# Kernel optimization log

Hardware: AMD Instinct MI355X
Metric: run time of the kernel (lower is better)

The kernel has to match this reference:

```python
import jax, jax.numpy as jnp
import numpy as np

B, C, H_IMG, W_IMG = 8, 256, 32, 32
KS, VS, NH = 64, 64, 8
DIM_HEAD = KS * NH  # 512
S = H_IMG * W_IMG   # 1024


def _conv1x1(x, w, b):
    # x: (B, Cin, H, W), w: (Cout, Cin), b: (Cout,)
    return jnp.einsum('oc,bchw->bohw', w, x) + b[None, :, None, None]


def _gated_resnet(x, w1, b1, w2, b2):
    # kernel_size=1, no aux/cond/norm/dropout -> conv1(elu(x)); elu; conv2; GLU; +x
    h = _conv1x1(jax.nn.elu(x), w1, b1)
    h = _conv1x1(jax.nn.elu(h), w2, b2)
    a, g = jnp.split(h, 2, axis=1)
    return x + a * jax.nn.sigmoid(g)


def _branch(x, w1, b1, w2, b2, wn, bn):
    # GatedResNet followed by nin (1x1 linear over channels)
    return _conv1x1(_gated_resnet(x, w1, b1, w2, b2), wn, bn)


def setup_inputs() -> dict:
    key = jax.random.key(0)
    ks = jax.random.split(key, 16)
    d = {}
    d['query'] = jax.random.normal(ks[0], (B, C, H_IMG, W_IMG), jnp.float32)
    d['key'] = jax.random.normal(ks[1], (B, C, H_IMG, W_IMG), jnp.float32)
    i = 2
    for p, out_dim in [('q', DIM_HEAD), ('k', DIM_HEAD), ('v', VS * NH)]:
        d[f'{p}_gr_w1'] = jax.random.normal(ks[i], (C, C), jnp.float32) * 0.05; i += 1
        d[f'{p}_gr_b1'] = jnp.zeros((C,), jnp.float32)
        d[f'{p}_gr_w2'] = jax.random.normal(ks[i], (2 * C, C), jnp.float32) * 0.05; i += 1
        d[f'{p}_gr_b2'] = jnp.zeros((2 * C,), jnp.float32)
        d[f'{p}_nin_w'] = jax.random.normal(ks[i], (out_dim, C), jnp.float32) * 0.05; i += 1
        d[f'{p}_nin_b'] = jnp.zeros((out_dim,), jnp.float32)
    return d


def reference(query, key,
              q_gr_w1, q_gr_b1, q_gr_w2, q_gr_b2, q_nin_w, q_nin_b,
              k_gr_w1, k_gr_b1, k_gr_w2, k_gr_b2, k_nin_w, k_nin_b,
              v_gr_w1, v_gr_b1, v_gr_w2, v_gr_b2, v_nin_w, v_nin_b):
    b, _, h, w = key.shape
    s = h * w
    q = _branch(query, q_gr_w1, q_gr_b1, q_gr_w2, q_gr_b2, q_nin_w, q_nin_b)  # (B, NH*KS, H, W)
    v = _branch(key, v_gr_w1, v_gr_b1, v_gr_w2, v_gr_b2, v_nin_w, v_nin_b)    # (B, NH*VS, H, W)
    k = _branch(key, k_gr_w1, k_gr_b1, k_gr_w2, k_gr_b2, k_nin_w, k_nin_b)    # (B, NH*KS, H, W)

    # Faithful to torch .view on contiguous NCHW (row-major reshape mixes C and HW)
    q = q.reshape(b, -1, NH, KS).swapaxes(1, 2)          # (B, NH, S, KS)
    k = k.reshape(b, -1, NH, KS).transpose(0, 2, 3, 1)   # (B, NH, KS, S)
    v = v.reshape(b, -1, NH, VS).swapaxes(1, 2)          # (B, NH, S, VS)

    attn = jnp.matmul(q, k) / jnp.sqrt(jnp.float32(DIM_HEAD))  # (B, NH, S, S)
    # mask = triu(ones, k=1).T -> strictly lower triangular allowed (diagonal masked)
    allowed = jnp.tril(jnp.ones((s, s), bool), k=-1)
    attn = jnp.where(allowed, attn, jnp.float32(-10000.0))
    attn = jax.nn.softmax(attn, axis=3)
    # start_mask zeros out the first query row
    start_mask = jnp.ones((s, 1), jnp.float32).at[0, 0].set(0.0)
    attn = attn * start_mask

    out = jnp.matmul(attn, v)                 # (B, NH, S, VS)
    out = out.swapaxes(1, 2).reshape(b, h, w, VS * NH)
    out = out.transpose(0, 3, 1, 2)           # (B, VS*NH, H, W)
    return out
```

## Files before the change

kernel.cpp:

```cpp
#include <hip/hip_runtime.h>
#include <cstdint>
#include <cstddef>

typedef __attribute__((ext_vector_type(4))) float f32x4;
typedef __attribute__((ext_vector_type(8))) short bf16x8;
typedef __attribute__((ext_vector_type(4))) short bf16x4;
typedef __attribute__((ext_vector_type(2))) short bf16x2;

#define DEVI static __device__ __forceinline__

DEVI short f2bf(float f){
  union { float f; uint32_t u; } v; v.f = f;
  uint32_t r = v.u + 0x7FFFu + ((v.u >> 16) & 1u);
  return (short)(r >> 16);
}
DEVI float bf2f(short h){
  union { uint32_t u; float f; } v; v.u = ((uint32_t)(uint16_t)h) << 16;
  return v.f;
}
DEVI float eluf(float x){ return x > 0.f ? x : (__expf(x) - 1.f); }
DEVI float sigm(float x){ return 1.f / (1.f + __expf(-x)); }

static constexpr int NPIX = 8 * 1024;

static constexpr size_t SZ_W   = (size_t)983040 * 2;
static constexpr size_t SZ_ACT = (size_t)NPIX * 256 * 2;
static constexpr size_t OFF_W   = 0;
static constexpr size_t OFF_TOK = OFF_W + SZ_W + 8*SZ_ACT;

__global__ void k_prep(const float* __restrict__ w1q, const float* __restrict__ w2q, const float* __restrict__ wnq,
                       const float* __restrict__ w1k, const float* __restrict__ w2k, const float* __restrict__ wnk,
                       const float* __restrict__ w1v, const float* __restrict__ w2v, const float* __restrict__ wnv,
                       short* __restrict__ dst)
{
  const float* s1[3] = {w1q, w1k, w1v};
  const float* s2[3] = {w2q, w2k, w2v};
  const float* s3[3] = {wnq, wnk, wnv};
  const int stride = gridDim.x * blockDim.x;
  for (int i = blockIdx.x * blockDim.x + threadIdx.x; i < 983040; i += stride){
    int br = i / 327680;
    int r  = i - br * 327680;
    float v;
    if (r < 65536)        v = s1[br][r];
    else if (r < 196608)  v = s2[br][r - 65536];
    else                  v = s3[br][r - 196608];
    dst[i] = f2bf(v);
  }
}

DEVI const short* stage_ptr(const short* W1z, int s, int& r0){
  if (s < 8){ r0 = s << 5; return W1z; }
  if (s < 24){ int t = s - 8; r0 = ((t & 2) << 7) + ((t >> 2) << 6) + ((t & 1) << 5); return W1z + 65536; }
  int t = s - 24; r0 = t << 5; return W1z + 196608;
}

__global__ __launch_bounds__(256, 2)
void k_branch(const short* __restrict__ wsW,
              const float* __restrict__ query, const float* __restrict__ key,
              const float* __restrict__ b1q, const float* __restrict__ b1k, const float* __restrict__ b1v,
              const float* __restrict__ b2q, const float* __restrict__ b2k, const float* __restrict__ b2v,
              const float* __restrict__ bnq, const float* __restrict__ bnk, const float* __restrict__ bnv,
              short* __restrict__ tok)
{
  __shared__ short sW[2][8192];
  __shared__ short sHG[4][4096];

  const int z = blockIdx.y;
  const float* xin = (z == 0) ? query : key;
  const float* b1z = (z == 0) ? b1q : ((z == 1) ? b1k : b1v);
  const float* b2z = (z == 0) ? b2q : ((z == 1) ? b2k : b2v);
  const float* bnz = (z == 0) ? bnq : ((z == 1) ? bnk : bnv);
  const short* W1 = wsW + (size_t)z * 327680;
  short* tokz = tok + (size_t)z * NPIX * 512;

  const int tid = threadIdx.x, w = tid >> 6, g = (tid >> 4) & 3, li = tid & 15;
  const int gtok = blockIdx.x * 64 + w * 16;
  const int b = gtok >> 10, s0 = gtok & 1023;
  short* sHw = &sHG[w][0];
  const float* xb = xin + (size_t)b * 256 * 1024;

  bf16x8 stg[4];
#define STAGE_ISSUE(SN)                                                         \
  { int r0_; const short* Wb_ = stage_ptr(W1, (SN), r0_);                       \
    _Pragma("unroll")                                                           \
    for (int it = 0; it < 4; it++){                                             \
      int gi = tid + it*256;                                                    \
      stg[it] = *(const bf16x8*)(Wb_ + (size_t)(r0_ + (gi >> 5))*256 + ((gi & 31) << 3)); } }
#define STAGE_WRITE(BUF)                                                        \
  { _Pragma("unroll")                                                           \
    for (int it = 0; it < 4; it++){                                             \
      int gi = tid + it*256; int row = gi >> 5;                                 \
      *(bf16x8*)((BUF) + row*256 + ((((gi & 31) ^ (row & 7))) << 3)) = stg[it]; } }

  STAGE_ISSUE(0);
  STAGE_WRITE(sW[0]);

  bf16x8 bB[8];
  #pragma unroll
  for (int ks = 0; ks < 8; ks++){
    #pragma unroll
    for (int j = 0; j < 8; j++){
      float e = xb[(size_t)(ks*32 + g*8 + j)*1024 + s0 + li];
      bB[ks][j] = f2bf(eluf(e));
    }
  }

  for (int s = 0; s < 8; s++){
    __syncthreads();
    STAGE_ISSUE(s + 1);
    const short* bufc = sW[s & 1];
    f32x4 acc[2] = {};
    #pragma unroll
    for (int mt = 0; mt < 2; mt++)
      #pragma unroll
      for (int ks = 0; ks < 8; ks++){
        bf16x8 afr = *(const bf16x8*)(bufc + (mt*16 + li)*256 + (((ks*4 + g) ^ (li & 7)) << 3));
        acc[mt] = __builtin_amdgcn_mfma_f32_16x16x32_bf16(afr, bB[ks], acc[mt], 0, 0, 0);
      }
    #pragma unroll
    for (int mt = 0; mt < 2; mt++){
      int m0 = s*32 + mt*16 + g*4;
      bf16x4 pk;
      #pragma unroll
      for (int r = 0; r < 4; r++)
        pk[r] = f2bf(eluf(acc[mt][r] + b1z[m0 + r]));
      *(bf16x4*)(sHw + li*256 + (m0 ^ ((li & 7) << 3))) = pk;
    }
    STAGE_WRITE(sW[(s + 1) & 1]);
  }

  bf16x8 bH[8];
  #pragma unroll
  for (int ks = 0; ks < 8; ks++)
    bH[ks] = *(const bf16x8*)(sHw + li*256 + (((ks*4 + g) ^ (li & 7)) << 3));

  for (int mp = 0; mp < 4; mp++){
    f32x4 acc8[8] = {};
    #pragma unroll
    for (int q = 0; q < 4; q++){
      const int s = 8 + mp*4 + q;
      __syncthreads();
      STAGE_ISSUE(s + 1);
      const short* bufc = sW[s & 1];
      #pragma unroll
      for (int mt = 0; mt < 2; mt++)
        #pragma unroll
        for (int ks = 0; ks < 8; ks++){
          bf16x8 afr = *(const bf16x8*)(bufc + (mt*16 + li)*256 + (((ks*4 + g) ^ (li & 7)) << 3));
          acc8[q*2 + mt] = __builtin_amdgcn_mfma_f32_16x16x32_bf16(afr, bH[ks], acc8[q*2 + mt], 0, 0, 0);
        }
      STAGE_WRITE(sW[(s + 1) & 1]);
    }
    #pragma unroll
    for (int mt = 0; mt < 4; mt++){
      int m0 = mp*64 + mt*16 + g*4;
      bf16x4 pk;
      #pragma unroll
      for (int r = 0; r < 4; r++){
        float a  = acc8[mt][r] + b2z[m0 + r];
        float gg = acc8[4 + mt][r] + b2z[m0 + r + 256];
        float xv = xb[(size_t)(m0 + r)*1024 + s0 + li];
        pk[r] = f2bf(xv + a * sigm(gg));
      }
      *(bf16x4*)(sHw + li*256 + (m0 ^ ((li & 7) << 3))) = pk;
    }
  }

  bf16x8 bG[8];
  #pragma unroll
  for (int ks = 0; ks < 8; ks++)
    bG[ks] = *(const bf16x8*)(sHw + li*256 + (((ks*4 + g) ^ (li & 7)) << 3));

  for (int s3 = 0; s3 < 16; s3++){
    const int s = 24 + s3;
    __syncthreads();
    const int sn = (s + 1 < 40) ? (s + 1) : 39;
    STAGE_ISSUE(sn);
    const short* bufc = sW[s & 1];
    f32x4 acc[2] = {};
    #pragma unroll
    for (int mt = 0; mt < 2; mt++)
      #pragma unroll
      for (int ks = 0; ks < 8; ks++){
        bf16x8 afr = *(const bf16x8*)(bufc + (mt*16 + li)*256 + (((ks*4 + g) ^ (li & 7)) << 3));
        acc[mt] = __builtin_amdgcn_mfma_f32_16x16x32_bf16(afr, bG[ks], acc[mt], 0, 0, 0);
      }
    #pragma unroll
    for (int mt = 0; mt < 2; mt++){
      #pragma unroll
      for (int r = 0; r < 4; r++){
        int m = s3*32 + mt*16 + g*4 + r;
        tokz[((size_t)b*512 + m)*1024 + s0 + li] = f2bf(acc[mt][r] + bnz[m]);
      }
    }
    STAGE_WRITE(sW[(s + 1) & 1]);
  }
#undef STAGE_ISSUE
#undef STAGE_WRITE
}

__global__ void k_attn(const short* __restrict__ tok, float* __restrict__ out)
{
  const short* qtok = tok;
  const short* ktok = tok + (size_t)NPIX * 512;
  const short* vtok = tok + (size_t)2 * NPIX * 512;
  const int flat = blockIdx.x;
  const int p = flat >> 6;
  const int g4 = p >> 2, r4 = p & 3;
  const int qt = (g4 == 0) ? (15 - r4) : (g4 == 1) ? r4 : (g4 == 2) ? (11 - r4) : (4 + r4);
  const int bh = flat & 63;
  const int b = bh >> 3, nh = bh & 7;
  const int tid = threadIdx.x, lane = tid & 63, w = tid >> 6, g = (tid >> 4) & 3, li = tid & 15;
  const int qrow = qt*64 + w*16 + li;
  __shared__ short Kl[64*64];
  __shared__ short Vt[64*64];
  __shared__ short Pl[4][1024];

  const short* qptr = qtok + ((size_t)(b*1024 + qrow))*512 + nh*64;
  bf16x8 qf0 = *(const bf16x8*)(qptr + g*8);
  bf16x8 qf1 = *(const bf16x8*)(qptr + 32 + g*8);

  f32x4 accO[4] = {};
  float mrun = -1e30f, lrun = 0.f;
  const float scale = 0.04419417382415922f;
  short* Pw = &Pl[w][0];

  for (int kt = 0; kt <= qt; kt++){
    const int kb = kt * 64;
    __syncthreads();
    #pragma unroll
    for (int it = 0; it < 2; it++){
      int i = tid + it*256;
      int kr = i >> 3, kc = i & 7;
      bf16x8 v = *(const bf16x8*)(ktok + ((size_t)(b*1024 + kb + kr))*512 + nh*64 + kc*8);
      *(bf16x8*)(Kl + ((kr*64 + kc*8) ^ ((kr & 7) << 3))) = v;
    }
    #pragma unroll
    for (int it = 0; it < 2; it++){
      int d0 = w*8 + it*32;
      bf16x8 v = *(const bf16x8*)(vtok + ((size_t)(b*1024 + kb + lane))*512 + nh*64 + d0);
      #pragma unroll
      for (int j = 0; j < 8; j++){
        int d = d0 + j;
        Vt[(d*64 + lane) ^ ((d & 7) << 3)] = v[j];
      }
    }
    __syncthreads();

    float pv[16];
    float mt_ = -1e30f;
    const bool diag = (kt == qt);
    #pragma unroll
    for (int kf = 0; kf < 4; kf++){
      f32x4 sa = {};
      const int krow = kf*16 + li;
      bf16x8 ka  = *(const bf16x8*)(Kl + ((krow*64 + g*8) ^ ((krow & 7) << 3)));
      bf16x8 kbf = *(const bf16x8*)(Kl + ((krow*64 + 32 + g*8) ^ ((krow & 7) << 3)));
      sa = __builtin_amdgcn_mfma_f32_16x16x32_bf16(ka, qf0, sa, 0, 0, 0);
      sa = __builtin_amdgcn_mfma_f32_16x16x32_bf16(kbf, qf1, sa, 0, 0, 0);
      #pragma unroll
      for (int r = 0; r < 4; r++){
        const int keyg = kb + kf*16 + g*4 + r;
        float s = sa[r] * scale;
        const bool ok = (!diag) || (keyg < qrow);
        s = ok ? s : -1e30f;
        pv[kf*4 + r] = s;
        mt_ = fmaxf(mt_, s);
      }
    }
    mt_ = fmaxf(mt_, __shfl_xor(mt_, 16));
    mt_ = fmaxf(mt_, __shfl_xor(mt_, 32));
    const float mnew = fmaxf(mrun, mt_);
    const float alpha = __expf(mrun - mnew);
    short pr[16];
    float rs = 0.f;
    #pragma unroll
    for (int i2 = 0; i2 < 16; i2++){
      float p2 = (pv[i2] > -9e29f) ? __expf(pv[i2] - mnew) : 0.f;
      short pb = f2bf(p2);
      pr[i2] = pb;
      rs += bf2f(pb);
    }
    rs += __shfl_xor(rs, 16);
    rs += __shfl_xor(rs, 32);
    lrun = lrun * alpha + rs;
    mrun = mnew;
    #pragma unroll
    for (int df = 0; df < 4; df++){
      accO[df][0] *= alpha; accO[df][1] *= alpha;
      accO[df][2] *= alpha; accO[df][3] *= alpha;
    }
    #pragma unroll
    for (int kf = 0; kf < 4; kf++){
      #pragma unroll
      for (int rp = 0; rp < 2; rp++){
        bf16x2 two;
        two[0] = pr[kf*4 + rp*2];
        two[1] = pr[kf*4 + rp*2 + 1];
        const int key = kf*16 + g*4 + rp*2;
        *(bf16x2*)(Pw + ((li*64 + key) ^ ((li & 7) << 3))) = two;
      }
    }
    #pragma unroll
    for (int kc = 0; kc < 2; kc++){
      bf16x8 pf = *(const bf16x8*)(Pw + ((li*64 + kc*32 + g*8) ^ ((li & 7) << 3)));
      #pragma unroll
      for (int df = 0; df < 4; df++){
        const int dr = df*16 + li;
        bf16x8 vf = *(const bf16x8*)(Vt + ((dr*64 + kc*32 + g*8) ^ ((dr & 7) << 3)));
        accO[df] = __builtin_amdgcn_mfma_f32_16x16x32_bf16(vf, pf, accO[df], 0, 0, 0);
      }
    }
  }
  const float inv = (lrun > 0.f) ? (1.f / lrun) : 0.f;
  #pragma unroll
  for (int df = 0; df < 4; df++){
    #pragma unroll
    for (int r = 0; r < 4; r++){
      const int d = df*16 + g*4 + r;
      out[((size_t)b*512 + nh*64 + d)*1024 + qrow] = accO[df][r] * inv;
    }
  }
}

extern "C" void kernel_launch(void* const* d_in, const int* in_sizes, int n_in,
                              void* d_out, int out_size, void* d_ws, size_t ws_size,
                              hipStream_t stream)
{
  (void)in_sizes; (void)n_in; (void)out_size; (void)ws_size;
  const float* query = (const float*)d_in[0];
  const float* key   = (const float*)d_in[1];
  const float* w1[3] = {(const float*)d_in[2],  (const float*)d_in[8],  (const float*)d_in[14]};
  const float* b1[3] = {(const float*)d_in[3],  (const float*)d_in[9],  (const float*)d_in[15]};
  const float* w2[3] = {(const float*)d_in[4],  (const float*)d_in[10], (const float*)d_in[16]};
  const float* b2[3] = {(const float*)d_in[5],  (const float*)d_in[11], (const float*)d_in[17]};
  const float* wn[3] = {(const float*)d_in[6],  (const float*)d_in[12], (const float*)d_in[18]};
  const float* bn[3] = {(const float*)d_in[7],  (const float*)d_in[13], (const float*)d_in[19]};

  char* ws = (char*)d_ws;
  short* wsW = (short*)(ws + OFF_W);
  short* tok = (short*)(ws + OFF_TOK);
  float* out = (float*)d_out;

  k_prep<<<dim3(960), dim3(256), 0, stream>>>(w1[0], w2[0], wn[0],
                                              w1[1], w2[1], wn[1],
                                              w1[2], w2[2], wn[2], wsW);
  k_branch<<<dim3(128, 3), dim3(256), 0, stream>>>(wsW, query, key,
                                                   b1[0], b1[1], b1[2],
                                                   b2[0], b2[1], b2[2],
                                                   bn[0], bn[1], bn[2], tok);
  k_attn<<<dim3(1024), dim3(256), 0, stream>>>(tok, out);
}
```

Before: 81.05 us.

## Double tokens per wave in branch kernel and stream weights via global_load_lds

k_prep now writes weights pre-ordered by stage and pre-swizzled, so k_branch can copy each stage straight from global memory into LDS with global_load_lds, with no register staging. Each wave now handles 32 tokens instead of 16, so every weight fragment read from LDS feeds two MFMAs. This halves weight traffic per token and the grid shrinks to 64x3 blocks. In exchange there is more LDS and register use (launch bounds drop to 1 block per SM), fewer blocks to keep the GPU busy, and the barrier placement is reordered.

```diff
diff --git a/kernel.cpp b/kernel.cpp
--- a/kernel.cpp
+++ b/kernel.cpp
@@ -20,6 +20,11 @@
 }
 DEVI float eluf(float x){ return x > 0.f ? x : (__expf(x) - 1.f); }
 DEVI float sigm(float x){ return 1.f / (1.f + __expf(-x)); }
+
+DEVI void gload16(const void* g, void* l){
+  __builtin_amdgcn_global_load_lds((const __attribute__((address_space(1))) void*)g,
+                                   (__attribute__((address_space(3))) void*)l, 16, 0, 0);
+}
 
 static constexpr int NPIX = 8 * 1024;
 
@@ -36,25 +41,23 @@
   const float* s1[3] = {w1q, w1k, w1v};
   const float* s2[3] = {w2q, w2k, w2v};
   const float* s3[3] = {wnq, wnk, wnv};
-  const int stride = gridDim.x * blockDim.x;
-  for (int i = blockIdx.x * blockDim.x + threadIdx.x; i < 983040; i += stride){
-    int br = i / 327680;
-    int r  = i - br * 327680;
-    float v;
-    if (r < 65536)        v = s1[br][r];
-    else if (r < 196608)  v = s2[br][r - 65536];
-    else                  v = s3[br][r - 196608];
-    dst[i] = f2bf(v);
-  }
-}
-
-DEVI const short* stage_ptr(const short* W1z, int s, int& r0){
-  if (s < 8){ r0 = s << 5; return W1z; }
-  if (s < 24){ int t = s - 8; r0 = ((t & 2) << 7) + ((t >> 2) << 6) + ((t & 1) << 5); return W1z + 65536; }
-  int t = s - 24; r0 = t << 5; return W1z + 196608;
-}
-
-__global__ __launch_bounds__(256, 2)
+  int u = blockIdx.x * 256 + threadIdx.x;
+  if (u >= 122880) return;
+  int z = u / 40960, rem = u % 40960;
+  int stage = rem >> 10, rem2 = rem & 1023;
+  int r = rem2 >> 5, s_ = rem2 & 31;
+  int cslot = s_ ^ (r & 7);
+  const float* src; int row;
+  if (stage < 8){ src = s1[z]; row = stage*32 + r; }
+  else if (stage < 24){ int t = stage - 8; src = s2[z]; row = ((t&2)<<7) + ((t>>2)<<6) + ((t&1)<<5) + r; }
+  else { src = s3[z]; row = (stage-24)*32 + r; }
+  const float* p = src + (size_t)row*256 + cslot*8;
+  short* dq = dst + (size_t)u*8;
+  #pragma unroll
+  for (int e = 0; e < 8; e++) dq[e] = f2bf(p[e]);
+}
+
+__global__ __launch_bounds__(256, 1)
 void k_branch(const short* __restrict__ wsW,
               const float* __restrict__ query, const float* __restrict__ key,
               const float* __restrict__ b1q, const float* __restrict__ b1k, const float* __restrict__ b1v,
@@ -63,140 +66,149 @@
               short* __restrict__ tok)
 {
   __shared__ short sW[2][8192];
-  __shared__ short sHG[4][4096];
+  __shared__ short sHG[4][8192];
 
   const int z = blockIdx.y;
   const float* xin = (z == 0) ? query : key;
   const float* b1z = (z == 0) ? b1q : ((z == 1) ? b1k : b1v);
   const float* b2z = (z == 0) ? b2q : ((z == 1) ? b2k : b2v);
   const float* bnz = (z == 0) ? bnq : ((z == 1) ? bnk : bnv);
-  const short* W1 = wsW + (size_t)z * 327680;
+  const short* Wz = wsW + (size_t)z * 327680;
   short* tokz = tok + (size_t)z * NPIX * 512;
 
-  const int tid = threadIdx.x, w = tid >> 6, g = (tid >> 4) & 3, li = tid & 15;
-  const int gtok = blockIdx.x * 64 + w * 16;
-  const int b = gtok >> 10, s0 = gtok & 1023;
+  const int tid = threadIdx.x, w = tid >> 6, lane = tid & 63, g = (tid >> 4) & 3, li = tid & 15;
+  const int gtok = blockIdx.x * 128;
+  const int b = gtok >> 10;
+  const int sb = (gtok & 1023) + w*32;
   short* sHw = &sHG[w][0];
   const float* xb = xin + (size_t)b * 256 * 1024;
 
-  bf16x8 stg[4];
-#define STAGE_ISSUE(SN)                                                         \
-  { int r0_; const short* Wb_ = stage_ptr(W1, (SN), r0_);                       \
-    _Pragma("unroll")                                                           \
-    for (int it = 0; it < 4; it++){                                             \
-      int gi = tid + it*256;                                                    \
-      stg[it] = *(const bf16x8*)(Wb_ + (size_t)(r0_ + (gi >> 5))*256 + ((gi & 31) << 3)); } }
-#define STAGE_WRITE(BUF)                                                        \
-  { _Pragma("unroll")                                                           \
-    for (int it = 0; it < 4; it++){                                             \
-      int gi = tid + it*256; int row = gi >> 5;                                 \
-      *(bf16x8*)((BUF) + row*256 + ((((gi & 31) ^ (row & 7))) << 3)) = stg[it]; } }
-
-  STAGE_ISSUE(0);
-  STAGE_WRITE(sW[0]);
-
-  bf16x8 bB[8];
-  #pragma unroll
-  for (int ks = 0; ks < 8; ks++){
-    #pragma unroll
-    for (int j = 0; j < 8; j++){
-      float e = xb[(size_t)(ks*32 + g*8 + j)*1024 + s0 + li];
-      bB[ks][j] = f2bf(eluf(e));
-    }
-  }
+#define STAGE(S, NB)                                                            \
+  { const char* gs_ = (const char*)(Wz + (size_t)(S)*8192) + w*4096 + lane*16;  \
+    char* ls_ = (char*)&sW[(NB)][0] + w*4096;                                   \
+    gload16(gs_,        ls_);                                                   \
+    gload16(gs_ + 1024, ls_ + 1024);                                            \
+    gload16(gs_ + 2048, ls_ + 2048);                                            \
+    gload16(gs_ + 3072, ls_ + 3072); }
+
+  STAGE(0, 0);
+
+  bf16x8 bB[2][8];
+  #pragma unroll
+  for (int th = 0; th < 2; th++)
+    #pragma unroll
+    for (int ks = 0; ks < 8; ks++)
+      #pragma unroll
+      for (int j = 0; j < 8; j++){
+        float e = xb[(size_t)(ks*32 + g*8 + j)*1024 + sb + th*16 + li];
+        bB[th][ks][j] = f2bf(eluf(e));
+      }
+  __syncthreads();
 
   for (int s = 0; s < 8; s++){
+    STAGE(s + 1, (s + 1) & 1);
+    const short* bufc = &sW[s & 1][0];
+    f32x4 acc[2][2] = {};
+    #pragma unroll
+    for (int ks = 0; ks < 8; ks++)
+      #pragma unroll
+      for (int mt = 0; mt < 2; mt++){
+        bf16x8 afr = *(const bf16x8*)(bufc + (mt*16 + li)*256 + (((ks*4 + g) ^ (li & 7)) << 3));
+        #pragma unroll
+        for (int th = 0; th < 2; th++)
+          acc[th][mt] = __builtin_amdgcn_mfma_f32_16x16x32_bf16(afr, bB[th][ks], acc[th][mt], 0, 0, 0);
+      }
+    #pragma unroll
+    for (int th = 0; th < 2; th++)
+      #pragma unroll
+      for (int mt = 0; mt < 2; mt++){
+        int m0 = s*32 + mt*16 + g*4;
+        bf16x4 pk;
+        #pragma unroll
+        for (int r = 0; r < 4; r++)
+          pk[r] = f2bf(eluf(acc[th][mt][r] + b1z[m0 + r]));
+        *(bf16x4*)(sHw + (th*16 + li)*256 + (m0 ^ ((li & 7) << 3))) = pk;
+      }
     __syncthreads();
-    STAGE_ISSUE(s + 1);
-    const short* bufc = sW[s & 1];
-    f32x4 acc[2] = {};
-    #pragma unroll
-    for (int mt = 0; mt < 2; mt++)
-      #pragma unroll
-      for (int ks = 0; ks < 8; ks++){
-        bf16x8 afr = *(const bf16x8*)(bufc + (mt*16 + li)*256 + (((ks*4 + g) ^ (li & 7)) << 3));
-        acc[mt] = __builtin_amdgcn_mfma_f32_16x16x32_bf16(afr, bB[ks], acc[mt], 0, 0, 0);
-      }
-    #pragma unroll
-    for (int mt = 0; mt < 2; mt++){
-      int m0 = s*32 + mt*16 + g*4;
-      bf16x4 pk;
-      #pragma unroll
-      for (int r = 0; r < 4; r++)
-        pk[r] = f2bf(eluf(acc[mt][r] + b1z[m0 + r]));
-      *(bf16x4*)(sHw + li*256 + (m0 ^ ((li & 7) << 3))) = pk;
-    }
-    STAGE_WRITE(sW[(s + 1) & 1]);
-  }
-
-  bf16x8 bH[8];
-  #pragma unroll
-  for (int ks = 0; ks < 8; ks++)
-    bH[ks] = *(const bf16x8*)(sHw + li*256 + (((ks*4 + g) ^ (li & 7)) << 3));
+  }
+
+  bf16x8 bH[2][8];
+  #pragma unroll
+  for (int th = 0; th < 2; th++)
+    #pragma unroll
+    for (int ks = 0; ks < 8; ks++)
+      bH[th][ks] = *(const bf16x8*)(sHw + (th*16 + li)*256 + (((ks*4 + g) ^ (li & 7)) << 3));
 
   for (int mp = 0; mp < 4; mp++){
-    f32x4 acc8[8] = {};
+    f32x4 acc2[2][8] = {};
     #pragma unroll
     for (int q = 0; q < 4; q++){
       const int s = 8 + mp*4 + q;
+      STAGE(s + 1, (s + 1) & 1);
+      const short* bufc = &sW[s & 1][0];
+      #pragma unroll
+      for (int ks = 0; ks < 8; ks++)
+        #pragma unroll
+        for (int mt = 0; mt < 2; mt++){
+          bf16x8 afr = *(const bf16x8*)(bufc + (mt*16 + li)*256 + (((ks*4 + g) ^ (li & 7)) << 3));
+          #pragma unroll
+          for (int th = 0; th < 2; th++)
+            acc2[th][q*2 + mt] = __builtin_amdgcn_mfma_f32_16x16x32_bf16(afr, bH[th][ks], acc2[th][q*2 + mt], 0, 0, 0);
+        }
       __syncthreads();
-      STAGE_ISSUE(s + 1);
-      const short* bufc = sW[s & 1];
-      #pragma unroll
-      for (int mt = 0; mt < 2; mt++)
-        #pragma unroll
-        for (int ks = 0; ks < 8; ks++){
-          bf16x8 afr = *(const bf16x8*)(bufc + (mt*16 + li)*256 + (((ks*4 + g) ^ (li & 7)) << 3));
-          acc8[q*2 + mt] = __builtin_amdgcn_mfma_f32_16x16x32_bf16(afr, bH[ks], acc8[q*2 + mt], 0, 0, 0);
+    }
+    #pragma unroll
+    for (int th = 0; th < 2; th++)
+      #pragma unroll
+      for (int q = 0; q < 2; q++)
+        #pragma unroll
+        for (int mt = 0; mt < 2; mt++){
+          int m0 = mp*64 + q*32 + mt*16 + g*4;
+          bf16x4 pk;
+          #pragma unroll
+          for (int r = 0; r < 4; r++){
+            float a  = acc2[th][q*2 + mt][r] + b2z[m0 + r];
+            float gg = acc2[th][q*2 + mt + 4][r] + b2z[m0 + r + 256];
+            float xv = xb[(size_t)(m0 + r)*1024 + sb + th*16 + li];
+            pk[r] = f2bf(xv + a * sigm(gg));
+          }
+          *(bf16x4*)(sHw + (th*16 + li)*256 + (m0 ^ ((li & 7) << 3))) = pk;
         }
-      STAGE_WRITE(sW[(s + 1) & 1]);
-    }
-    #pragma unroll
-    for (int mt = 0; mt < 4; mt++){
-      int m0 = mp*64 + mt*16 + g*4;
-      bf16x4 pk;
-      #pragma unroll
-      for (int r = 0; r < 4; r++){
-        float a  = acc8[mt][r] + b2z[m0 + r];
-        float gg = acc8[4 + mt][r] + b2z[m0 + r + 256];
-        float xv = xb[(size_t)(m0 + r)*1024 + s0 + li];
-        pk[r] = f2bf(xv + a * sigm(gg));
-      }
-      *(bf16x4*)(sHw + li*256 + (m0 ^ ((li & 7) << 3))) = pk;
-    }
-  }
-
-  bf16x8 bG[8];
-  #pragma unroll
-  for (int ks = 0; ks < 8; ks++)
-    bG[ks] = *(const bf16x8*)(sHw + li*256 + (((ks*4 + g) ^ (li & 7)) << 3));
+  }
+
+  bf16x8 bG[2][8];
+  #pragma unroll
+  for (int th = 0; th < 2; th++)
+    #pragma unroll
+    for (int ks = 0; ks < 8; ks++)
+      bG[th][ks] = *(const bf16x8*)(sHw + (th*16 + li)*256 + (((ks*4 + g) ^ (li & 7)) << 3));
 
   for (int s3 = 0; s3 < 16; s3++){
     const int s = 24 + s3;
-    __syncthreads();
-    const int sn = (s + 1 < 40) ? (s + 1) : 39;
-    STAGE_ISSUE(sn);
-    const short* bufc = sW[s & 1];
-    f32x4 acc[2] = {};
-    #pragma unroll
-    for (int mt = 0; mt < 2; mt++)
-      #pragma unroll
-      for (int ks = 0; ks < 8; ks++){
+    if (s + 1 < 40) STAGE(s + 1, (s + 1) & 1);
+    const short* bufc = &sW[s & 1][0];
+    f32x4 acc[2][2] = {};
+    #pragma unroll
+    for (int ks = 0; ks < 8; ks++)
+      #pragma unroll
+      for (int mt = 0; mt < 2; mt++){
         bf16x8 afr = *(const bf16x8*)(bufc + (mt*16 + li)*256 + (((ks*4 + g) ^ (li & 7)) << 3));
-        acc[mt] = __builtin_amdgcn_mfma_f32_16x16x32_bf16(afr, bG[ks], acc[mt], 0, 0, 0);
-      }
-    #pragma unroll
-    for (int mt = 0; mt < 2; mt++){
-      #pragma unroll
-      for (int r = 0; r < 4; r++){
-        int m = s3*32 + mt*16 + g*4 + r;
-        tokz[((size_t)b*512 + m)*1024 + s0 + li] = f2bf(acc[mt][r] + bnz[m]);
-      }
-    }
-    STAGE_WRITE(sW[(s + 1) & 1]);
-  }
-#undef STAGE_ISSUE
-#undef STAGE_WRITE
+        #pragma unroll
+        for (int th = 0; th < 2; th++)
+          acc[th][mt] = __builtin_amdgcn_mfma_f32_16x16x32_bf16(afr, bG[th][ks], acc[th][mt], 0, 0, 0);
+      }
+    #pragma unroll
+    for (int th = 0; th < 2; th++)
+      #pragma unroll
+      for (int mt = 0; mt < 2; mt++)
+        #pragma unroll
+        for (int r = 0; r < 4; r++){
+          int m = s3*32 + mt*16 + g*4 + r;
+          tokz[((size_t)b*512 + m)*1024 + sb + th*16 + li] = f2bf(acc[th][mt][r] + bnz[m]);
+        }
+    if (s + 1 < 40) __syncthreads();
+  }
+#undef STAGE
 }
 
 __global__ void k_attn(const short* __restrict__ tok, float* __restrict__ out)
@@ -342,12 +354,12 @@
   short* tok = (short*)(ws + OFF_TOK);
   float* out = (float*)d_out;
 
-  k_prep<<<dim3(960), dim3(256), 0, stream>>>(w1[0], w2[0], wn[0],
+  k_prep<<<dim3(480), dim3(256), 0, stream>>>(w1[0], w2[0], wn[0],
                                               w1[1], w2[1], wn[1],
                                               w1[2], w2[2], wn[2], wsW);
-  k_branch<<<dim3(128, 3), dim3(256), 0, stream>>>(wsW, query, key,
-                                                   b1[0], b1[1], b1[2],
-                                                   b2[0], b2[1], b2[2],
-                                                   bn[0], bn[1], bn[2], tok);
+  k_branch<<<dim3(64, 3), dim3(256), 0, stream>>>(wsW, query, key,
+                                                  b1[0], b1[1], b1[2],
+                                                  b2[0], b2[1], b2[2],
+                                                  bn[0], bn[1], bn[2], tok);
   k_attn<<<dim3(1024), dim3(256), 0, stream>>>(tok, out);
 }
```

Result: slower. 104.3 us (+28.7%).

## Restructure branch MLP kernel: register-tile weights from global, activations in shared

Applied to the files above, without the earlier changes.

The branch kernel used to stream weight chunks through a double-buffered shared-memory pipeline, with each wave holding its own 16 tokens in registers. It now stages the block's 64-token activation tile in shared memory using vectorized coalesced input loads and a transpose. Each wave computes a 64-row output slice over all 64 tokens with 4x4 MFMA register tiles, reading weight fragments directly from global memory (L2). This removes most of the per-stage barriers and the weight staging, and raises MFMA reuse per fragment load. In exchange it depends on global or L2 latency for the weight reads and has higher register pressure.

```diff
diff --git a/kernel.cpp b/kernel.cpp
--- a/kernel.cpp
+++ b/kernel.cpp
@@ -48,12 +48,6 @@
   }
 }
 
-DEVI const short* stage_ptr(const short* W1z, int s, int& r0){
-  if (s < 8){ r0 = s << 5; return W1z; }
-  if (s < 24){ int t = s - 8; r0 = ((t & 2) << 7) + ((t >> 2) << 6) + ((t & 1) << 5); return W1z + 65536; }
-  int t = s - 24; r0 = t << 5; return W1z + 196608;
-}
-
 __global__ __launch_bounds__(256, 2)
 void k_branch(const short* __restrict__ wsW,
               const float* __restrict__ query, const float* __restrict__ key,
@@ -62,8 +56,8 @@
               const float* __restrict__ bnq, const float* __restrict__ bnk, const float* __restrict__ bnv,
               short* __restrict__ tok)
 {
-  __shared__ short sW[2][8192];
-  __shared__ short sHG[4][4096];
+  __shared__ short sB0[64*256];
+  __shared__ short sB1[64*256];
 
   const int z = blockIdx.y;
   const float* xin = (z == 0) ? query : key;
@@ -71,132 +65,153 @@
   const float* b2z = (z == 0) ? b2q : ((z == 1) ? b2k : b2v);
   const float* bnz = (z == 0) ? bnq : ((z == 1) ? bnk : bnv);
   const short* W1 = wsW + (size_t)z * 327680;
+  const short* W2 = W1 + 65536;
+  const short* Wn = W1 + 196608;
   short* tokz = tok + (size_t)z * NPIX * 512;
 
   const int tid = threadIdx.x, w = tid >> 6, g = (tid >> 4) & 3, li = tid & 15;
-  const int gtok = blockIdx.x * 64 + w * 16;
-  const int b = gtok >> 10, s0 = gtok & 1023;
-  short* sHw = &sHG[w][0];
+  const int bx = blockIdx.x, b = bx >> 4, sp0 = (bx & 15) * 64;
   const float* xb = xin + (size_t)b * 256 * 1024;
-
-  bf16x8 stg[4];
-#define STAGE_ISSUE(SN)                                                         \
-  { int r0_; const short* Wb_ = stage_ptr(W1, (SN), r0_);                       \
-    _Pragma("unroll")                                                           \
-    for (int it = 0; it < 4; it++){                                             \
-      int gi = tid + it*256;                                                    \
-      stg[it] = *(const bf16x8*)(Wb_ + (size_t)(r0_ + (gi >> 5))*256 + ((gi & 31) << 3)); } }
-#define STAGE_WRITE(BUF)                                                        \
-  { _Pragma("unroll")                                                           \
-    for (int it = 0; it < 4; it++){                                             \
-      int gi = tid + it*256; int row = gi >> 5;                                 \
-      *(bf16x8*)((BUF) + row*256 + ((((gi & 31) ^ (row & 7))) << 3)) = stg[it]; } }
-
-  STAGE_ISSUE(0);
-  STAGE_WRITE(sW[0]);
-
-  bf16x8 bB[8];
+  const int sw = (li & 7) << 3;
+
   #pragma unroll
-  for (int ks = 0; ks < 8; ks++){
-    #pragma unroll
-    for (int j = 0; j < 8; j++){
-      float e = xb[(size_t)(ks*32 + g*8 + j)*1024 + s0 + li];
-      bB[ks][j] = f2bf(eluf(e));
-    }
-  }
-
-  for (int s = 0; s < 8; s++){
-    __syncthreads();
-    STAGE_ISSUE(s + 1);
-    const short* bufc = sW[s & 1];
-    f32x4 acc[2] = {};
+  for (int i = 0; i < 16; i++){
+    int idx = tid + i*256;
+    int c = idx >> 4, u = idx & 15;
+    f32x4 v4 = *(const f32x4*)(xb + (size_t)c*1024 + sp0 + u*4);
+    bf16x4 pk;
+    #pragma unroll
+    for (int r = 0; r < 4; r++) pk[r] = f2bf(eluf(v4[r]));
+    *(bf16x4*)(sB1 + c*64 + u*4) = pk;
+  }
+  __syncthreads();
+  #pragma unroll
+  for (int i = 0; i < 8; i++){
+    int idx = tid + i*256;
+    int t = idx & 63, cb = idx >> 6;
+    bf16x8 pk;
+    #pragma unroll
+    for (int j = 0; j < 8; j++) pk[j] = sB1[(cb*8 + j)*64 + t];
+    *(bf16x8*)(sB0 + t*256 + ((cb*8) ^ (((t & 7)) << 3))) = pk;
+  }
+  __syncthreads();
+
+  {
+    f32x4 bias[4];
+    #pragma unroll
+    for (int mt = 0; mt < 4; mt++)
+      bias[mt] = *(const f32x4*)(b1z + w*64 + mt*16 + g*4);
+    f32x4 acc[4][4] = {};
+    #pragma unroll
+    for (int ks = 0; ks < 8; ks++){
+      bf16x8 Af[4], Bf[4];
+      #pragma unroll
+      for (int mt = 0; mt < 4; mt++)
+        Af[mt] = *(const bf16x8*)(W1 + (size_t)(w*64 + mt*16 + li)*256 + ks*32 + g*8);
+      #pragma unroll
+      for (int nt = 0; nt < 4; nt++)
+        Bf[nt] = *(const bf16x8*)(sB0 + (nt*16 + li)*256 + ((ks*32 + g*8) ^ sw));
+      #pragma unroll
+      for (int mt = 0; mt < 4; mt++)
+        #pragma unroll
+        for (int nt = 0; nt < 4; nt++)
+          acc[mt][nt] = __builtin_amdgcn_mfma_f32_16x16x32_bf16(Af[mt], Bf[nt], acc[mt][nt], 0, 0, 0);
+    }
+    #pragma unroll
+    for (int mt = 0; mt < 4; mt++)
+      #pragma unroll
+      for (int nt = 0; nt < 4; nt++){
+        bf16x4 pk;
+        #pragma unroll
+        for (int r = 0; r < 4; r++)
+          pk[r] = f2bf(eluf(acc[mt][nt][r] + bias[mt][r]));
+        *(bf16x4*)(sB1 + (nt*16 + li)*256 + ((w*64 + mt*16 + g*4) ^ sw)) = pk;
+      }
+  }
+  __syncthreads();
+
+  #pragma unroll 1
+  for (int p = 0; p < 2; p++){
+    f32x4 ba[2], bg[2];
+    #pragma unroll
+    for (int mt = 0; mt < 2; mt++){
+      ba[mt] = *(const f32x4*)(b2z + w*64 + p*32 + mt*16 + g*4);
+      bg[mt] = *(const f32x4*)(b2z + 256 + w*64 + p*32 + mt*16 + g*4);
+    }
+    float xr[2][4][4];
     #pragma unroll
     for (int mt = 0; mt < 2; mt++)
       #pragma unroll
-      for (int ks = 0; ks < 8; ks++){
-        bf16x8 afr = *(const bf16x8*)(bufc + (mt*16 + li)*256 + (((ks*4 + g) ^ (li & 7)) << 3));
-        acc[mt] = __builtin_amdgcn_mfma_f32_16x16x32_bf16(afr, bB[ks], acc[mt], 0, 0, 0);
-      }
-    #pragma unroll
-    for (int mt = 0; mt < 2; mt++){
-      int m0 = s*32 + mt*16 + g*4;
-      bf16x4 pk;
-      #pragma unroll
-      for (int r = 0; r < 4; r++)
-        pk[r] = f2bf(eluf(acc[mt][r] + b1z[m0 + r]));
-      *(bf16x4*)(sHw + li*256 + (m0 ^ ((li & 7) << 3))) = pk;
-    }
-    STAGE_WRITE(sW[(s + 1) & 1]);
-  }
-
-  bf16x8 bH[8];
-  #pragma unroll
-  for (int ks = 0; ks < 8; ks++)
-    bH[ks] = *(const bf16x8*)(sHw + li*256 + (((ks*4 + g) ^ (li & 7)) << 3));
-
-  for (int mp = 0; mp < 4; mp++){
-    f32x4 acc8[8] = {};
-    #pragma unroll
-    for (int q = 0; q < 4; q++){
-      const int s = 8 + mp*4 + q;
-      __syncthreads();
-      STAGE_ISSUE(s + 1);
-      const short* bufc = sW[s & 1];
-      #pragma unroll
-      for (int mt = 0; mt < 2; mt++)
-        #pragma unroll
-        for (int ks = 0; ks < 8; ks++){
-          bf16x8 afr = *(const bf16x8*)(bufc + (mt*16 + li)*256 + (((ks*4 + g) ^ (li & 7)) << 3));
-          acc8[q*2 + mt] = __builtin_amdgcn_mfma_f32_16x16x32_bf16(afr, bH[ks], acc8[q*2 + mt], 0, 0, 0);
+      for (int nt = 0; nt < 4; nt++)
+        #pragma unroll
+        for (int r = 0; r < 4; r++)
+          xr[mt][nt][r] = xb[(size_t)(w*64 + p*32 + mt*16 + g*4 + r)*1024 + sp0 + nt*16 + li];
+    f32x4 aa[2][4] = {}, ag[2][4] = {};
+    #pragma unroll
+    for (int ks = 0; ks < 8; ks++){
+      bf16x8 Bf[4];
+      #pragma unroll
+      for (int nt = 0; nt < 4; nt++)
+        Bf[nt] = *(const bf16x8*)(sB1 + (nt*16 + li)*256 + ((ks*32 + g*8) ^ sw));
+      #pragma unroll
+      for (int mt = 0; mt < 2; mt++){
+        bf16x8 Aa = *(const bf16x8*)(W2 + (size_t)(w*64 + p*32 + mt*16 + li)*256 + ks*32 + g*8);
+        bf16x8 Ag = *(const bf16x8*)(W2 + (size_t)(256 + w*64 + p*32 + mt*16 + li)*256 + ks*32 + g*8);
+        #pragma unroll
+        for (int nt = 0; nt < 4; nt++){
+          aa[mt][nt] = __builtin_amdgcn_mfma_f32_16x16x32_bf16(Aa, Bf[nt], aa[mt][nt], 0, 0, 0);
+          ag[mt][nt] = __builtin_amdgcn_mfma_f32_16x16x32_bf16(Ag, Bf[nt], ag[mt][nt], 0, 0, 0);
         }
-      STAGE_WRITE(sW[(s + 1) & 1]);
-    }
-    #pragma unroll
-    for (int mt = 0; mt < 4; mt++){
-      int m0 = mp*64 + mt*16 + g*4;
-      bf16x4 pk;
-      #pragma unroll
-      for (int r = 0; r < 4; r++){
-        float a  = acc8[mt][r] + b2z[m0 + r];
-        float gg = acc8[4 + mt][r] + b2z[m0 + r + 256];
-        float xv = xb[(size_t)(m0 + r)*1024 + s0 + li];
-        pk[r] = f2bf(xv + a * sigm(gg));
-      }
-      *(bf16x4*)(sHw + li*256 + (m0 ^ ((li & 7) << 3))) = pk;
-    }
-  }
-
-  bf16x8 bG[8];
-  #pragma unroll
-  for (int ks = 0; ks < 8; ks++)
-    bG[ks] = *(const bf16x8*)(sHw + li*256 + (((ks*4 + g) ^ (li & 7)) << 3));
-
-  for (int s3 = 0; s3 < 16; s3++){
-    const int s = 24 + s3;
-    __syncthreads();
-    const int sn = (s + 1 < 40) ? (s + 1) : 39;
-    STAGE_ISSUE(sn);
-    const short* bufc = sW[s & 1];
-    f32x4 acc[2] = {};
+      }
+    }
     #pragma unroll
     for (int mt = 0; mt < 2; mt++)
       #pragma unroll
-      for (int ks = 0; ks < 8; ks++){
-        bf16x8 afr = *(const bf16x8*)(bufc + (mt*16 + li)*256 + (((ks*4 + g) ^ (li & 7)) << 3));
-        acc[mt] = __builtin_amdgcn_mfma_f32_16x16x32_bf16(afr, bG[ks], acc[mt], 0, 0, 0);
-      }
-    #pragma unroll
-    for (int mt = 0; mt < 2; mt++){
-      #pragma unroll
-      for (int r = 0; r < 4; r++){
-        int m = s3*32 + mt*16 + g*4 + r;
-        tokz[((size_t)b*512 + m)*1024 + s0 + li] = f2bf(acc[mt][r] + bnz[m]);
-      }
-    }
-    STAGE_WRITE(sW[(s + 1) & 1]);
-  }
-#undef STAGE_ISSUE
-#undef STAGE_WRITE
+      for (int nt = 0; nt < 4; nt++){
+        bf16x4 pk;
+        #pragma unroll
+        for (int r = 0; r < 4; r++){
+          float a  = aa[mt][nt][r] + ba[mt][r];
+          float gg = ag[mt][nt][r] + bg[mt][r];
+          pk[r] = f2bf(xr[mt][nt][r] + a * sigm(gg));
+        }
+        *(bf16x4*)(sB0 + (nt*16 + li)*256 + ((w*64 + p*32 + mt*16 + g*4) ^ sw)) = pk;
+      }
+  }
+  __syncthreads();
+
+  #pragma unroll 1
+  for (int p = 0; p < 2; p++){
+    f32x4 bias[4];
+    #pragma unroll
+    for (int mt = 0; mt < 4; mt++)
+      bias[mt] = *(const f32x4*)(bnz + w*128 + p*64 + mt*16 + g*4);
+    f32x4 acc[4][4] = {};
+    #pragma unroll
+    for (int ks = 0; ks < 8; ks++){
+      bf16x8 Af[4], Bf[4];
+      #pragma unroll
+      for (int mt = 0; mt < 4; mt++)
+        Af[mt] = *(const bf16x8*)(Wn + (size_t)(w*128 + p*64 + mt*16 + li)*256 + ks*32 + g*8);
+      #pragma unroll
+      for (int nt = 0; nt < 4; nt++)
+        Bf[nt] = *(const bf16x8*)(sB0 + (nt*16 + li)*256 + ((ks*32 + g*8) ^ sw));
+      #pragma unroll
+      for (int mt = 0; mt < 4; mt++)
+        #pragma unroll
+        for (int nt = 0; nt < 4; nt++)
+          acc[mt][nt] = __builtin_amdgcn_mfma_f32_16x16x32_bf16(Af[mt], Bf[nt], acc[mt][nt], 0, 0, 0);
+    }
+    #pragma unroll
+    for (int mt = 0; mt < 4; mt++)
+      #pragma unroll
+      for (int nt = 0; nt < 4; nt++)
+        #pragma unroll
+        for (int r = 0; r < 4; r++){
+          int m = w*128 + p*64 + mt*16 + g*4 + r;
+          tokz[((size_t)b*512 + m)*1024 + sp0 + nt*16 + li] = f2bf(acc[mt][nt][r] + bias[mt][r]);
+        }
+  }
 }
 
 __global__ void k_attn(const short* __restrict__ tok, float* __restrict__ out)
```

After: 109.1 us. 1.35x slower.
